# Optimization experiments

Measured on AMD Instinct MI355X. Metric: run time of the kernel, lower is better.

## Reference

```python
import jax, jax.numpy as jnp
import numpy as np

L = 3
EPSILON = 0.01
T = 1.0
L1_EPS = 1e-12  # torch F.normalize default eps


def _cdist(x, y):
    # Euclidean pairwise distance, (b, n, d) x (b, m, d) -> (b, n, m)
    x2 = jnp.sum(x * x, axis=-1, keepdims=True)            # (b, n, 1)
    y2 = jnp.sum(y * y, axis=-1)[:, None, :]               # (b, 1, m)
    xy = jnp.einsum('bnd,bmd->bnm', x, y)                  # (b, n, m)
    return jnp.sqrt(jnp.maximum(x2 + y2 - 2.0 * xy, 0.0))


def setup_inputs() -> dict:
    key = jax.random.key(0)
    k1, k2 = jax.random.split(key)
    B, S, D = 4, 2048, 512
    A = jax.random.uniform(k1, (B, S, S), dtype=jnp.float32)
    V = jax.random.normal(k2, (B, S, D), dtype=jnp.float32)
    return {"A": A, "V": V}


def reference(A, V):
    M = jnp.matmul(A, V)  # (b, s, d)
    for _ in range(L):
        Md = jax.lax.stop_gradient(M)
        Vd = jax.lax.stop_gradient(V)
        dist = _cdist(Md, Vd)                               # (b, s, s)
        w = 1.0 / (dist + EPSILON)                          # norm == 'L2'
        ww = w * A                                          # (b, s, s)
        l1 = jnp.maximum(jnp.sum(jnp.abs(ww), axis=-1, keepdims=True), L1_EPS)
        ww_norm = ww / l1
        M = (1.0 - T) * M + T * jnp.matmul(ww_norm, V)
    return M
```

## Files before the change

kernel.cpp:

```cpp
#include <hip/hip_runtime.h>


typedef __bf16 bf16;
typedef bf16 bf16x4 __attribute__((ext_vector_type(4)));
typedef bf16 bf16x8 __attribute__((ext_vector_type(8)));
typedef float f32x4 __attribute__((ext_vector_type(4)));

#define S_DIM 2048
#define D_DIM 512
#define NB    4
#define EPSILON 0.01f

__global__ void cast_kernel(const float* __restrict__ in, bf16* __restrict__ out, int n4) {
  int i = blockIdx.x * blockDim.x + threadIdx.x;
  if (i >= n4) return;
  float4 v = ((const float4*)in)[i];
  bf16x4 o = { (bf16)v.x, (bf16)v.y, (bf16)v.z, (bf16)v.w };
  ((bf16x4*)out)[i] = o;
}

__global__ void vprep_kernel(const float* __restrict__ V, bf16* __restrict__ Vbf,
                             bf16* __restrict__ Vt) {
  __shared__ float tile[64][68];
  int b  = blockIdx.z;
  int c0 = blockIdx.x * 64;
  int r0 = blockIdx.y * 64;
  const float* Vb = V   + (size_t)b * S_DIM * D_DIM;
  bf16*       Vfb = Vbf + (size_t)b * S_DIM * D_DIM;
  bf16*       Vtb = Vt  + (size_t)b * S_DIM * D_DIM;
  int tx = threadIdx.x & 15, ty = threadIdx.x >> 4;
#pragma unroll
  for (int i = 0; i < 4; ++i) {
    int r = ty + i * 16;
    float4 v = *(const float4*)(Vb + (size_t)(r0 + r) * D_DIM + (c0 + tx * 4));
    tile[r][tx * 4 + 0] = v.x; tile[r][tx * 4 + 1] = v.y;
    tile[r][tx * 4 + 2] = v.z; tile[r][tx * 4 + 3] = v.w;
    bf16x4 o = { (bf16)v.x, (bf16)v.y, (bf16)v.z, (bf16)v.w };
    *(bf16x4*)(Vfb + (size_t)(r0 + r) * D_DIM + (c0 + tx * 4)) = o;
  }
  __syncthreads();
#pragma unroll
  for (int i = 0; i < 4; ++i) {
    int c = ty + i * 16;
    bf16x4 o = { (bf16)tile[tx * 4 + 0][c], (bf16)tile[tx * 4 + 1][c],
                 (bf16)tile[tx * 4 + 2][c], (bf16)tile[tx * 4 + 3][c] };
    *(bf16x4*)(Vtb + (size_t)(c0 + c) * S_DIM + (r0 + tx * 4)) = o;
  }
}

__global__ void rownorm_kernel(const bf16* __restrict__ X, float* __restrict__ out) {
  int row  = blockIdx.x * 4 + (threadIdx.x >> 6);
  int lane = threadIdx.x & 63;
  bf16x8 v = *(const bf16x8*)(X + (size_t)row * D_DIM + lane * 8);
  float s = 0.f;
#pragma unroll
  for (int i = 0; i < 8; ++i) { float f = (float)v[i]; s += f * f; }
#pragma unroll
  for (int off = 32; off > 0; off >>= 1) s += __shfl_down(s, off);
  if (lane == 0) out[row] = s;
}

template <int MODE>
__global__ __launch_bounds__(256, 4)
void gemm_kernel(const bf16* __restrict__ Amat, const bf16* __restrict__ Bmat,
                 int M, int N, int K,
                 bf16* __restrict__ Cp,
                 const float* __restrict__ m2, const float* __restrict__ v2,
                 const bf16* __restrict__ Aw, bf16* __restrict__ Wout,
                 float* __restrict__ l1p) {
  int bz, ks, kbeg, kend;
  if (MODE == 4) { bz = blockIdx.z >> 1; ks = blockIdx.z & 1; kbeg = ks * (K >> 1); kend = kbeg + (K >> 1); }
  else           { bz = blockIdx.z;      ks = 0;              kbeg = 0;             kend = K; }
  const int row0 = blockIdx.y * 128;
  const int col0 = blockIdx.x * 128;
  const bf16* Ab = Amat + (size_t)bz * M * K;
  const bf16* Bb = Bmat + (size_t)bz * N * K;

  __shared__ char smem[32768];
  bf16*  ldsA = (bf16*)smem;
  bf16*  ldsB = (bf16*)(smem + 16384);
  float* ldsW = (float*)smem;

  const int tid  = threadIdx.x;
  const int wave = tid >> 6;
  const int lane = tid & 63;
  const int wr   = wave >> 1;
  const int wc   = wave & 1;
  const int q    = lane >> 4;
  const int c16  = lane & 15;

  const int srow = lane >> 3;
  const int scol = ((lane & 7) ^ srow) * 8;

  f32x4 acc[4][4] = {};

  for (int k0 = kbeg; k0 < kend; k0 += 64) {
#pragma unroll
    for (int i = 0; i < 4; ++i) {
      int slot = wave * 4 + i;
      int r = slot * 8 + srow;
      __builtin_amdgcn_global_load_lds(
          (const __attribute__((address_space(1))) void*)(Ab + (size_t)(row0 + r) * K + (k0 + scol)),
          (__attribute__((address_space(3))) void*)(ldsA + slot * 512), 16, 0, 0);
      __builtin_amdgcn_global_load_lds(
          (const __attribute__((address_space(1))) void*)(Bb + (size_t)(col0 + r) * K + (k0 + scol)),
          (__attribute__((address_space(3))) void*)(ldsB + slot * 512), 16, 0, 0);
    }
    __syncthreads();

#pragma unroll
    for (int kk = 0; kk < 2; ++kk) {
      bf16x8 afr[4], bfr[4];
#pragma unroll
      for (int mt = 0; mt < 4; ++mt) {
        int R = wr * 64 + mt * 16 + c16;
        int p = ((kk << 2) + q) ^ (c16 & 7);
        afr[mt] = *(const bf16x8*)(ldsA + (size_t)R * 64 + p * 8);
      }
#pragma unroll
      for (int nt = 0; nt < 4; ++nt) {
        int R = wc * 64 + nt * 16 + c16;
        int p = ((kk << 2) + q) ^ (c16 & 7);
        bfr[nt] = *(const bf16x8*)(ldsB + (size_t)R * 64 + p * 8);
      }
#pragma unroll
      for (int mt = 0; mt < 4; ++mt)
#pragma unroll
        for (int nt = 0; nt < 4; ++nt)
          acc[mt][nt] = __builtin_amdgcn_mfma_f32_16x16x32_bf16(afr[mt], bfr[nt], acc[mt][nt], 0, 0, 0);
    }
    __syncthreads();
  }

  const int rowBase = row0 + wr * 64 + q * 4;
  const int colBase = col0 + wc * 64 + c16;

  if (MODE == 1) {
    const float* m2b = m2 + (size_t)bz * M;
    const float* v2b = v2 + (size_t)bz * N;
    float v2v[4];
#pragma unroll
    for (int nt = 0; nt < 4; ++nt) v2v[nt] = v2b[colBase + nt * 16];
#pragma unroll
    for (int mt = 0; mt < 4; ++mt)
#pragma unroll
      for (int r = 0; r < 4; ++r) {
        float m2v = m2b[rowBase + mt * 16 + r];
#pragma unroll
        for (int nt = 0; nt < 4; ++nt) {
          float d2 = fmaxf(m2v + v2v[nt] - 2.f * acc[mt][nt][r], 0.f);
          acc[mt][nt][r] = __builtin_amdgcn_rcpf(__builtin_amdgcn_sqrtf(d2) + EPSILON);
        }
      }
  }

  const int lr  = tid >> 3;
  const int sub = tid & 7;
#pragma unroll
  for (int k = 0; k < 4; ++k) {
    __syncthreads();
    if (wr == (k >> 1)) {
#pragma unroll
      for (int m = 0; m < 2; ++m) {
        int mt = 2 * (k & 1) + m;
#pragma unroll
        for (int nt = 0; nt < 4; ++nt)
#pragma unroll
          for (int r = 0; r < 4; ++r)
            ldsW[(m * 16 + q * 4 + r) * 132 + wc * 64 + nt * 16 + c16] = acc[mt][nt][r];
      }
    }
    __syncthreads();
    int gi = row0 + 32 * k + lr;
    const float* wp = ldsW + lr * 132 + sub * 16;
    float4 w0 = *(const float4*)(wp + 0);
    float4 w1 = *(const float4*)(wp + 4);
    float4 w2 = *(const float4*)(wp + 8);
    float4 w3 = *(const float4*)(wp + 12);
    float wv_[16] = { w0.x, w0.y, w0.z, w0.w, w1.x, w1.y, w1.z, w1.w,
                      w2.x, w2.y, w2.z, w2.w, w3.x, w3.y, w3.z, w3.w };
    if (MODE == 1) {
      const bf16* ap = Aw + (size_t)bz * M * N + (size_t)gi * N + (col0 + sub * 16);
      bf16x8 a0 = *(const bf16x8*)(ap);
      bf16x8 a1 = *(const bf16x8*)(ap + 8);
      bf16x8 o0, o1;
      float rs = 0.f;
#pragma unroll
      for (int e = 0; e < 8; ++e) {
        float x0 = wv_[e] * (float)a0[e];
        float x1 = wv_[e + 8] * (float)a1[e];
        o0[e] = (bf16)x0; o1[e] = (bf16)x1;
        rs += fabsf(x0) + fabsf(x1);
      }
      bf16* op = Wout + (size_t)bz * M * N + (size_t)gi * N + (col0 + sub * 16);
      *(bf16x8*)(op)     = o0;
      *(bf16x8*)(op + 8) = o1;
      rs += __shfl_xor(rs, 1);
      rs += __shfl_xor(rs, 2);
      rs += __shfl_xor(rs, 4);
      if (sub == 0) l1p[((size_t)blockIdx.x * NB + bz) * M + gi] = rs;
    } else {
      bf16* Cb = Cp + ((size_t)ks * NB + bz) * ((size_t)M * N);
      bf16x8 o0, o1;
#pragma unroll
      for (int e = 0; e < 8; ++e) { o0[e] = (bf16)wv_[e]; o1[e] = (bf16)wv_[e + 8]; }
      bf16* op = Cb + (size_t)gi * N + (col0 + sub * 16);
      *(bf16x8*)(op)     = o0;
      *(bf16x8*)(op + 8) = o1;
    }
  }
}

template <int RMODE>
__global__ void reduce_kernel(const bf16* __restrict__ part, const float* __restrict__ l1p,
                              bf16* __restrict__ Mo, float* __restrict__ Fo,
                              float* __restrict__ m2) {
  int wave = threadIdx.x >> 6, lane = threadIdx.x & 63;
  int rg = blockIdx.x * 4 + wave;
  const bf16* p0 = part + (size_t)rg * D_DIM + lane * 8;
  const bf16* p1 = p0 + (size_t)NB * S_DIM * D_DIM;
  bf16x8 a = *(const bf16x8*)p0;
  bf16x8 b = *(const bf16x8*)p1;
  float v[8];
#pragma unroll
  for (int e = 0; e < 8; ++e) v[e] = (float)a[e] + (float)b[e];
  float sc = 1.f;
  if (RMODE >= 1) {
    int bb = rg >> 11, row = rg & (S_DIM - 1);
    float l1v = 0.f;
#pragma unroll
    for (int e = 0; e < 16; ++e) l1v += l1p[((size_t)e * NB + bb) * S_DIM + row];
    sc = __builtin_amdgcn_rcpf(fmaxf(l1v, 1e-12f));
  }
  float s = 0.f;
#pragma unroll
  for (int e = 0; e < 8; ++e) { v[e] *= sc; s += v[e] * v[e]; }
  if (RMODE == 2) {
    float4 o0 = { v[0], v[1], v[2], v[3] }, o1 = { v[4], v[5], v[6], v[7] };
    float* op = Fo + (size_t)rg * D_DIM + lane * 8;
    *(float4*)(op) = o0; *(float4*)(op + 4) = o1;
  } else {
    bf16x8 o;
#pragma unroll
    for (int e = 0; e < 8; ++e) o[e] = (bf16)v[e];
    *(bf16x8*)(Mo + (size_t)rg * D_DIM + lane * 8) = o;
#pragma unroll
    for (int off = 32; off > 0; off >>= 1) s += __shfl_xor(s, off);
    if (lane == 0) m2[rg] = s;
  }
}

extern "C" void kernel_launch(void* const* d_in, const int* in_sizes, int n_in,
                              void* d_out, int out_size, void* d_ws, size_t ws_size,
                              hipStream_t stream) {
  const float* A = (const float*)d_in[0];
  const float* V = (const float*)d_in[1];
  float* out = (float*)d_out;

  char* ws = (char*)d_ws;
  bf16* Abf = (bf16*)ws;   ws += (size_t)NB * S_DIM * S_DIM * 2;
  bf16* Vbf = (bf16*)ws;   ws += (size_t)NB * S_DIM * D_DIM * 2;
  bf16* Vt  = (bf16*)ws;   ws += (size_t)NB * S_DIM * D_DIM * 2;
  bf16* Mbf = (bf16*)ws;   ws += (size_t)NB * S_DIM * D_DIM * 2;
  bf16* Wbf = (bf16*)ws;   ws += (size_t)NB * S_DIM * S_DIM * 2;
  bf16* part = (bf16*)ws;  ws += (size_t)2 * NB * S_DIM * D_DIM * 2;
  float* v2 = (float*)ws;  ws += (size_t)NB * S_DIM * 4;
  float* m2 = (float*)ws;  ws += (size_t)NB * S_DIM * 4;
  float* l1p = (float*)ws; ws += (size_t)16 * NB * S_DIM * 4;

  int nA4 = NB * S_DIM * S_DIM / 4;
  cast_kernel<<<nA4 / 256, 256, 0, stream>>>(A, Abf, nA4);
  vprep_kernel<<<dim3(D_DIM / 64, S_DIM / 64, NB), 256, 0, stream>>>(V, Vbf, Vt);
  rownorm_kernel<<<NB * S_DIM / 4, 256, 0, stream>>>(Vbf, v2);

  gemm_kernel<4><<<dim3(D_DIM / 128, S_DIM / 128, NB * 2), 256, 0, stream>>>(
      Abf, Vt, S_DIM, D_DIM, S_DIM, part, nullptr, nullptr, nullptr, nullptr, nullptr);
  reduce_kernel<0><<<NB * S_DIM / 4, 256, 0, stream>>>(part, nullptr, Mbf, nullptr, m2);

  for (int it = 0; it < 3; ++it) {
    gemm_kernel<1><<<dim3(S_DIM / 128, S_DIM / 128, NB), 256, 0, stream>>>(
        Mbf, Vbf, S_DIM, S_DIM, D_DIM, nullptr, m2, v2, Abf, Wbf, l1p);
    gemm_kernel<4><<<dim3(D_DIM / 128, S_DIM / 128, NB * 2), 256, 0, stream>>>(
        Wbf, Vt, S_DIM, D_DIM, S_DIM, part, nullptr, nullptr, nullptr, nullptr, nullptr);
    if (it < 2)
      reduce_kernel<1><<<NB * S_DIM / 4, 256, 0, stream>>>(part, l1p, Mbf, nullptr, m2);
    else
      reduce_kernel<2><<<NB * S_DIM / 4, 256, 0, stream>>>(part, l1p, nullptr, out, nullptr);
  }
}
```

Measured before the change: 339.4 us.

## Double-buffer GEMM LDS staging with BK=32 and fuse V row norms into vprep

The GEMM main loop changes from a single 64-wide K tile with two barriers per step to two 32-wide K buffers. The next tile is prefetched by global_load_lds while the current one feeds MFMA, with one barrier per iteration. The XOR swizzle on LDS reads is dropped, which risks bank conflicts, and each K step now carries half as many MFMAs per barrier. The separate rownorm kernel is removed: vprep now computes squared row norms with shuffles and atomics, and a memset clears v2 first.

```diff
diff --git a/kernel.cpp b/kernel.cpp
--- a/kernel.cpp
+++ b/kernel.cpp
@@ -20,7 +20,7 @@
 }
 
 __global__ void vprep_kernel(const float* __restrict__ V, bf16* __restrict__ Vbf,
-                             bf16* __restrict__ Vt) {
+                             bf16* __restrict__ Vt, float* __restrict__ v2) {
   __shared__ float tile[64][68];
   int b  = blockIdx.z;
   int c0 = blockIdx.x * 64;
@@ -28,6 +28,7 @@
   const float* Vb = V   + (size_t)b * S_DIM * D_DIM;
   bf16*       Vfb = Vbf + (size_t)b * S_DIM * D_DIM;
   bf16*       Vtb = Vt  + (size_t)b * S_DIM * D_DIM;
+  float*      v2b = v2  + (size_t)b * S_DIM;
   int tx = threadIdx.x & 15, ty = threadIdx.x >> 4;
 #pragma unroll
   for (int i = 0; i < 4; ++i) {
@@ -37,6 +38,12 @@
     tile[r][tx * 4 + 2] = v.z; tile[r][tx * 4 + 3] = v.w;
     bf16x4 o = { (bf16)v.x, (bf16)v.y, (bf16)v.z, (bf16)v.w };
     *(bf16x4*)(Vfb + (size_t)(r0 + r) * D_DIM + (c0 + tx * 4)) = o;
+    float s = 0.f;
+#pragma unroll
+    for (int j = 0; j < 4; ++j) { float f = (float)o[j]; s += f * f; }
+    s += __shfl_xor(s, 1); s += __shfl_xor(s, 2);
+    s += __shfl_xor(s, 4); s += __shfl_xor(s, 8);
+    if (tx == 0) atomicAdd(&v2b[r0 + r], s);
   }
   __syncthreads();
 #pragma unroll
@@ -46,18 +53,6 @@
                  (bf16)tile[tx * 4 + 2][c], (bf16)tile[tx * 4 + 3][c] };
     *(bf16x4*)(Vtb + (size_t)(c0 + c) * S_DIM + (r0 + tx * 4)) = o;
   }
-}
-
-__global__ void rownorm_kernel(const bf16* __restrict__ X, float* __restrict__ out) {
-  int row  = blockIdx.x * 4 + (threadIdx.x >> 6);
-  int lane = threadIdx.x & 63;
-  bf16x8 v = *(const bf16x8*)(X + (size_t)row * D_DIM + lane * 8);
-  float s = 0.f;
-#pragma unroll
-  for (int i = 0; i < 8; ++i) { float f = (float)v[i]; s += f * f; }
-#pragma unroll
-  for (int off = 32; off > 0; off >>= 1) s += __shfl_down(s, off);
-  if (lane == 0) out[row] = s;
 }
 
 template <int MODE>
@@ -77,8 +72,6 @@
   const bf16* Bb = Bmat + (size_t)bz * N * K;
 
   __shared__ char smem[32768];
-  bf16*  ldsA = (bf16*)smem;
-  bf16*  ldsB = (bf16*)(smem + 16384);
   float* ldsW = (float*)smem;
 
   const int tid  = threadIdx.x;
@@ -89,47 +82,48 @@
   const int q    = lane >> 4;
   const int c16  = lane & 15;
 
-  const int srow = lane >> 3;
-  const int scol = ((lane & 7) ^ srow) * 8;
-
-  f32x4 acc[4][4] = {};
-
-  for (int k0 = kbeg; k0 < kend; k0 += 64) {
-#pragma unroll
-    for (int i = 0; i < 4; ++i) {
-      int slot = wave * 4 + i;
-      int r = slot * 8 + srow;
+  const int srow = lane >> 2;
+  const int scol = (lane & 3) * 8;
+
+  auto stage = [&](int buf, int k0) {
+    bf16* dA = (bf16*)(smem + buf * 16384);
+    bf16* dB = (bf16*)(smem + buf * 16384 + 8192);
+#pragma unroll
+    for (int i = 0; i < 2; ++i) {
+      int slot = wave * 2 + i;
+      int r = slot * 16 + srow;
       __builtin_amdgcn_global_load_lds(
           (const __attribute__((address_space(1))) void*)(Ab + (size_t)(row0 + r) * K + (k0 + scol)),
-          (__attribute__((address_space(3))) void*)(ldsA + slot * 512), 16, 0, 0);
+          (__attribute__((address_space(3))) void*)(dA + slot * 512), 16, 0, 0);
       __builtin_amdgcn_global_load_lds(
           (const __attribute__((address_space(1))) void*)(Bb + (size_t)(col0 + r) * K + (k0 + scol)),
-          (__attribute__((address_space(3))) void*)(ldsB + slot * 512), 16, 0, 0);
+          (__attribute__((address_space(3))) void*)(dB + slot * 512), 16, 0, 0);
     }
+  };
+
+  f32x4 acc[4][4] = {};
+
+  const int nIter = (kend - kbeg) >> 5;
+  stage(0, kbeg);
+  for (int it = 0; it < nIter; ++it) {
+    const int cur = it & 1;
     __syncthreads();
-
-#pragma unroll
-    for (int kk = 0; kk < 2; ++kk) {
-      bf16x8 afr[4], bfr[4];
-#pragma unroll
-      for (int mt = 0; mt < 4; ++mt) {
-        int R = wr * 64 + mt * 16 + c16;
-        int p = ((kk << 2) + q) ^ (c16 & 7);
-        afr[mt] = *(const bf16x8*)(ldsA + (size_t)R * 64 + p * 8);
-      }
-#pragma unroll
-      for (int nt = 0; nt < 4; ++nt) {
-        int R = wc * 64 + nt * 16 + c16;
-        int p = ((kk << 2) + q) ^ (c16 & 7);
-        bfr[nt] = *(const bf16x8*)(ldsB + (size_t)R * 64 + p * 8);
-      }
-#pragma unroll
-      for (int mt = 0; mt < 4; ++mt)
-#pragma unroll
-        for (int nt = 0; nt < 4; ++nt)
-          acc[mt][nt] = __builtin_amdgcn_mfma_f32_16x16x32_bf16(afr[mt], bfr[nt], acc[mt][nt], 0, 0, 0);
-    }
-    __syncthreads();
+    if (it + 1 < nIter)
+      stage(cur ^ 1, kbeg + ((it + 1) << 5));
+    const bf16* lA = (const bf16*)(smem + cur * 16384);
+    const bf16* lB = (const bf16*)(smem + cur * 16384 + 8192);
+    bf16x8 afr[4], bfr[4];
+#pragma unroll
+    for (int mt = 0; mt < 4; ++mt)
+      afr[mt] = *(const bf16x8*)(lA + (size_t)(wr * 64 + mt * 16 + c16) * 32 + q * 8);
+#pragma unroll
+    for (int nt = 0; nt < 4; ++nt)
+      bfr[nt] = *(const bf16x8*)(lB + (size_t)(wc * 64 + nt * 16 + c16) * 32 + q * 8);
+#pragma unroll
+    for (int mt = 0; mt < 4; ++mt)
+#pragma unroll
+      for (int nt = 0; nt < 4; ++nt)
+        acc[mt][nt] = __builtin_amdgcn_mfma_f32_16x16x32_bf16(afr[mt], bfr[nt], acc[mt][nt], 0, 0, 0);
   }
 
   const int rowBase = row0 + wr * 64 + q * 4;
@@ -270,8 +264,8 @@
 
   int nA4 = NB * S_DIM * S_DIM / 4;
   cast_kernel<<<nA4 / 256, 256, 0, stream>>>(A, Abf, nA4);
-  vprep_kernel<<<dim3(D_DIM / 64, S_DIM / 64, NB), 256, 0, stream>>>(V, Vbf, Vt);
-  rownorm_kernel<<<NB * S_DIM / 4, 256, 0, stream>>>(Vbf, v2);
+  hipMemsetAsync(v2, 0, (size_t)NB * S_DIM * 4, stream);
+  vprep_kernel<<<dim3(D_DIM / 64, S_DIM / 64, NB), 256, 0, stream>>>(V, Vbf, Vt, v2);
 
   gemm_kernel<4><<<dim3(D_DIM / 128, S_DIM / 128, NB * 2), 256, 0, stream>>>(
       Abf, Vt, S_DIM, D_DIM, S_DIM, part, nullptr, nullptr, nullptr, nullptr, nullptr);
```

After: 351.0 us. +3.4%, slower.
